# Performance work log

Measured on AMD Instinct MI355X. Metric: run time of the kernel, lower is better.

The kernel has to match this reference:

```python
import jax, jax.numpy as jnp
import numpy as np
from jax import lax

NUM_CLASSES = 2
LINE_THRESHOLD = 300.0


def _maxpool3x3(x):
    # x: [B, H, W]; PyTorch max_pool2d(kernel=3, stride=1, padding=1) pads with -inf
    return lax.reduce_window(x, -jnp.inf, lax.max,
                             window_dimensions=(1, 3, 3),
                             window_strides=(1, 1, 1),
                             padding=((0, 0), (1, 1), (1, 1)))


def _remove_long_lines(b, threshold):
    # b: [B, H, W]. Zero rows whose sum >= threshold, THEN (on the modified
    # array, as in the original sequential numpy code) zero columns whose
    # sum >= threshold.
    row_hit = jnp.sum(b, axis=2) >= threshold          # [B, H]
    b = jnp.where(row_hit[:, :, None], 0.0, b)
    col_hit = jnp.sum(b, axis=1) >= threshold          # [B, W]
    b = jnp.where(col_hit[:, None, :], 0.0, b)
    return b


def _extract_boundary(gt_seg):
    # gt_seg: [B, H, W] float labels in {0, 1}
    boundary_mask = jnp.zeros_like(gt_seg)
    for k in range(NUM_CLASSES):
        mask = (gt_seg == k).astype(gt_seg.dtype)
        dilated = _maxpool3x3(mask)
        eroded = -_maxpool3x3(-mask)
        boundary = dilated - eroded
        boundary = _remove_long_lines(boundary, LINE_THRESHOLD)
        # Original skips empty classes, but an empty mask yields an all-zero
        # boundary, so unconditional accumulation is equivalent.
        boundary_mask = boundary_mask + boundary
    return boundary_mask


def setup_inputs() -> dict:
    key = jax.random.key(0)
    k1, k2 = jax.random.split(key)
    B, H, W = 64, 512, 512
    seg = jax.random.randint(k1, (B, H, W), 0, 2).astype(jnp.float32)
    gt = jax.random.randint(k2, (B, H, W), 0, 2).astype(jnp.float32)
    return {"seg": seg, "gt": gt}


def reference(seg, gt):
    pred_boundary = _extract_boundary(seg)
    gt_boundary = _extract_boundary(gt)
    return jnp.mean((pred_boundary - gt_boundary) ** 2)
```

## Files before the change

kernel.cpp:

```cpp
#include <hip/hip_runtime.h>
#include <cstdint>
#include <cstddef>

#define HH 512
#define WW 512
#define BB 64
#define RPW 16
#define STRIPS (HH / RPW)


__global__ __launch_bounds__(256) void boundary_bits_kernel(
    const float* __restrict__ seg, const float* __restrict__ gt,
    uint8_t* __restrict__ bits,
    unsigned long long* __restrict__ counter)
{
    if (blockIdx.x == 0 && threadIdx.x == 0) *counter = 0ull;

    const int lane  = threadIdx.x & 63;
    const int wid   = blockIdx.x * 4 + (threadIdx.x >> 6);
    const int z     = wid >> 11;
    const int rem   = wid & 2047;
    const int b     = rem >> 5;
    const int strip = rem & 31;
    const int r0    = strip * RPW;

    const float* img = (z ? gt : seg) + (size_t)b * HH * WW;
    uint8_t* brow = bits + (((size_t)z * BB + b) * HH) * 64;

    float hmx[3][8], hmn[3][8];

    auto loadrow = [&](int slot, int g) {
        if (unsigned(g) < (unsigned)HH) {
            const float* p = img + (size_t)g * WW + lane * 8;
            float4 va = *(const float4*)p;
            float4 vb = *(const float4*)(p + 4);
            int sl = (lane == 0) ? 0 : lane - 1;
            int sr = (lane == 63) ? 63 : lane + 1;
            float lf = __shfl(vb.w, sl); lf = (lane == 0)  ? va.x : lf;
            float rt = __shfl(va.x, sr); rt = (lane == 63) ? vb.w : rt;
            float e[10] = {lf, va.x, va.y, va.z, va.w, vb.x, vb.y, vb.z, vb.w, rt};
            #pragma unroll
            for (int c = 0; c < 8; ++c) {
                hmx[slot][c] = fmaxf(fmaxf(e[c], e[c + 1]), e[c + 2]);
                hmn[slot][c] = fminf(fminf(e[c], e[c + 1]), e[c + 2]);
            }
        } else {
            #pragma unroll
            for (int c = 0; c < 8; ++c) { hmx[slot][c] = -1e30f; hmn[slot][c] = 1e30f; }
        }
    };

    loadrow(0, r0 - 1);
    loadrow(1, r0);
    #pragma unroll
    for (int q = 0; q < RPW; ++q) {
        const int sP = q % 3, sC = (q + 1) % 3, sN = (q + 2) % 3;
        loadrow(sN, r0 + q + 1);
        unsigned byte = 0;
        #pragma unroll
        for (int c = 0; c < 8; ++c) {
            float wmax = fmaxf(fmaxf(hmx[sP][c], hmx[sC][c]), hmx[sN][c]);
            float wmin = fminf(fminf(hmn[sP][c], hmn[sC][c]), hmn[sN][c]);
            byte |= (wmax - wmin > 0.5f) ? (1u << c) : 0u;
        }
        brow[(size_t)(r0 + q) * 64 + lane] = (uint8_t)byte;
    }
}

__global__ __launch_bounds__(512) void colmask_xor_kernel(
    const uint64_t* __restrict__ bits,
    unsigned long long* __restrict__ counter)
{
    const int w   = blockIdx.x;
    const int b   = blockIdx.y;
    const int tid = threadIdx.x;
    const int wave = tid >> 6, lane = tid & 63;

    __shared__ unsigned int part[8][64];
    __shared__ unsigned long long cmaskS[2];
    __shared__ int red[8];

    uint64_t wd[2];
    #pragma unroll
    for (int z = 0; z < 2; ++z) {
        const uint64_t* bp = bits + ((size_t)z * BB + b) * HH * 8 + (size_t)tid * 8;
        uint64_t r[8];
        #pragma unroll
        for (int i = 0; i < 8; ++i) r[i] = bp[i];
        int rs = 0;
        #pragma unroll
        for (int i = 0; i < 8; ++i) rs += (int)__popcll(r[i]);
        uint64_t word = bp[w];
        word = (rs >= 300) ? 0ull : word;

        unsigned myp = 0;
        #pragma unroll
        for (int c = 0; c < 64; ++c) {
            unsigned long long m = __ballot((word >> c) & 1ull);
            if (lane == c) myp = (unsigned)__popcll(m);
        }
        part[wave][lane] = myp;
        __syncthreads();
        if (tid < 64) {
            int s = 0;
            #pragma unroll
            for (int v = 0; v < 8; ++v) s += part[v][tid];
            unsigned long long km = __ballot(s < 300);
            if (tid == 0) cmaskS[z] = km;
        }
        __syncthreads();
        wd[z] = word;
    }

    uint64_t x = (wd[0] & cmaskS[0]) ^ (wd[1] & cmaskS[1]);
    int cnt = (int)__popcll(x);
    #pragma unroll
    for (int off = 32; off; off >>= 1) cnt += __shfl_down(cnt, off);
    if (lane == 0) red[wave] = cnt;
    __syncthreads();
    if (tid == 0) {
        int s = 0;
        #pragma unroll
        for (int v = 0; v < 8; ++v) s += red[v];
        atomicAdd(counter, (unsigned long long)s);
    }
}

__global__ void finalize_kernel(const unsigned long long* __restrict__ counter,
                                float* __restrict__ out)
{
    if (threadIdx.x == 0 && blockIdx.x == 0) {
        double v = (double)(*counter) * (4.0 / 16777216.0);
        out[0] = (float)v;
    }
}

extern "C" void kernel_launch(void* const* d_in, const int* in_sizes, int n_in,
                              void* d_out, int out_size, void* d_ws, size_t ws_size,
                              hipStream_t stream) {
    const float* seg = (const float*)d_in[0];
    const float* gt  = (const float*)d_in[1];
    float* out = (float*)d_out;

    uint8_t* ws = (uint8_t*)d_ws;
    const size_t bits_bytes = (size_t)2 * BB * HH * 64;
    uint8_t* bits = ws;
    unsigned long long* counter = (unsigned long long*)(ws + bits_bytes);

    boundary_bits_kernel<<<1024, 256, 0, stream>>>(seg, gt, bits, counter);
    dim3 g2(8, BB);
    colmask_xor_kernel<<<g2, 512, 0, stream>>>((const uint64_t*)bits, counter);
    finalize_kernel<<<1, 1, 0, stream>>>(counter, out);
}
```

Measured before the change: 157.1 us.

## Fuse row-line removal into boundary kernel and restructure column-mask pass

The boundary kernel now zeroes long rows itself, using a wave-wide popcount reduction per row before storing the bit byte. The strip height is halved to launch twice as many waves, with an occupancy hint added. The column kernel now runs one block per image, where each wave accumulates full column counts for one 64-column word over all rows. This removes the redundant per-block row-sum reads and the second launch grid. In exchange, the column pass runs on only 64 blocks, each doing long serial ballot loops, which may underuse the GPU.

New measurement: 210.9 us. +34.2%, slower.

```diff
diff --git a/kernel.cpp b/kernel.cpp
--- a/kernel.cpp
+++ b/kernel.cpp
@@ -5,11 +5,11 @@
 #define HH 512
 #define WW 512
 #define BB 64
-#define RPW 16
+#define RPW 8
 #define STRIPS (HH / RPW)
 
 
-__global__ __launch_bounds__(256) void boundary_bits_kernel(
+__global__ __launch_bounds__(256, 8) void boundary_bits_kernel(
     const float* __restrict__ seg, const float* __restrict__ gt,
     uint8_t* __restrict__ bits,
     unsigned long long* __restrict__ counter)
@@ -18,10 +18,9 @@
 
     const int lane  = threadIdx.x & 63;
     const int wid   = blockIdx.x * 4 + (threadIdx.x >> 6);
-    const int z     = wid >> 11;
-    const int rem   = wid & 2047;
-    const int b     = rem >> 5;
-    const int strip = rem & 31;
+    const int z     = wid >> 12;
+    const int b     = (wid >> 6) & 63;
+    const int strip = wid & 63;
     const int r0    = strip * RPW;
 
     const float* img = (z ? gt : seg) + (size_t)b * HH * WW;
@@ -63,57 +62,53 @@
             float wmin = fminf(fminf(hmn[sP][c], hmn[sC][c]), hmn[sN][c]);
             byte |= (wmax - wmin > 0.5f) ? (1u << c) : 0u;
         }
+        int rs = __popc(byte);
+        #pragma unroll
+        for (int off = 32; off; off >>= 1) rs += __shfl_xor(rs, off);
+        byte = (rs >= 300) ? 0u : byte;
         brow[(size_t)(r0 + q) * 64 + lane] = (uint8_t)byte;
     }
 }
 
-__global__ __launch_bounds__(512) void colmask_xor_kernel(
+__global__ __launch_bounds__(512) void colxor_kernel(
     const uint64_t* __restrict__ bits,
     unsigned long long* __restrict__ counter)
 {
-    const int w   = blockIdx.x;
-    const int b   = blockIdx.y;
-    const int tid = threadIdx.x;
+    const int b    = blockIdx.x;
+    const int tid  = threadIdx.x;
     const int wave = tid >> 6, lane = tid & 63;
 
-    __shared__ unsigned int part[8][64];
-    __shared__ unsigned long long cmaskS[2];
+    __shared__ unsigned long long cmask[2][8];
     __shared__ int red[8];
 
-    uint64_t wd[2];
+    const int w = wave;
+    int cnt0 = 0, cnt1 = 0;
     #pragma unroll
     for (int z = 0; z < 2; ++z) {
-        const uint64_t* bp = bits + ((size_t)z * BB + b) * HH * 8 + (size_t)tid * 8;
-        uint64_t r[8];
+        const uint64_t* bb = bits + ((size_t)z * BB + b) * HH * 8;
         #pragma unroll
-        for (int i = 0; i < 8; ++i) r[i] = bp[i];
-        int rs = 0;
-        #pragma unroll
-        for (int i = 0; i < 8; ++i) rs += (int)__popcll(r[i]);
-        uint64_t word = bp[w];
-        word = (rs >= 300) ? 0ull : word;
+        for (int k = 0; k < 8; ++k) {
+            uint64_t word = bb[(size_t)(k * 64 + lane) * 8 + w];
+            #pragma unroll
+            for (int c = 0; c < 64; ++c) {
+                unsigned long long m = __ballot((word >> c) & 1ull);
+                int pc = __popcll(m);
+                if (lane == c) { if (z == 0) cnt0 += pc; else cnt1 += pc; }
+            }
+        }
+    }
+    unsigned long long km0 = __ballot(cnt0 < 300);
+    unsigned long long km1 = __ballot(cnt1 < 300);
+    if (lane == 0) { cmask[0][w] = km0; cmask[1][w] = km1; }
+    __syncthreads();
 
-        unsigned myp = 0;
-        #pragma unroll
-        for (int c = 0; c < 64; ++c) {
-            unsigned long long m = __ballot((word >> c) & 1ull);
-            if (lane == c) myp = (unsigned)__popcll(m);
-        }
-        part[wave][lane] = myp;
-        __syncthreads();
-        if (tid < 64) {
-            int s = 0;
-            #pragma unroll
-            for (int v = 0; v < 8; ++v) s += part[v][tid];
-            unsigned long long km = __ballot(s < 300);
-            if (tid == 0) cmaskS[z] = km;
-        }
-        __syncthreads();
-        wd[z] = word;
+    const uint64_t* bp = bits + ((size_t)0 * BB + b) * HH * 8 + (size_t)tid * 8;
+    const uint64_t* bg = bits + ((size_t)1 * BB + b) * HH * 8 + (size_t)tid * 8;
+    int cnt = 0;
+    #pragma unroll
+    for (int w2 = 0; w2 < 8; ++w2) {
+        cnt += (int)__popcll((bp[w2] & cmask[0][w2]) ^ (bg[w2] & cmask[1][w2]));
     }
-
-    uint64_t x = (wd[0] & cmaskS[0]) ^ (wd[1] & cmaskS[1]);
-    int cnt = (int)__popcll(x);
     #pragma unroll
     for (int off = 32; off; off >>= 1) cnt += __shfl_down(cnt, off);
     if (lane == 0) red[wave] = cnt;
@@ -147,8 +142,7 @@
     uint8_t* bits = ws;
     unsigned long long* counter = (unsigned long long*)(ws + bits_bytes);
 
-    boundary_bits_kernel<<<1024, 256, 0, stream>>>(seg, gt, bits, counter);
-    dim3 g2(8, BB);
-    colmask_xor_kernel<<<g2, 512, 0, stream>>>((const uint64_t*)bits, counter);
+    boundary_bits_kernel<<<2048, 256, 0, stream>>>(seg, gt, bits, counter);
+    colxor_kernel<<<BB, 512, 0, stream>>>((const uint64_t*)bits, counter);
     finalize_kernel<<<1, 1, 0, stream>>>(counter, out);
 }
```
